# Kernel optimization log

Hardware: AMD Instinct MI355X
Metric: run time of the kernel (lower is better)

## Reference

```python
import jax, jax.numpy as jnp
import numpy as np

D = 1024
H = 16
DH = D // H
DFF = 4096
EPS = 1e-5


def new_gelu(u):
    # HF NewGELUActivation: 0.5*u*(1+tanh(sqrt(2/pi)*(u+0.044715*u^3)))
    c = np.sqrt(2.0 / np.pi).astype(np.float32)
    return 0.5 * u * (1.0 + jnp.tanh(c * (u + 0.044715 * u ** 3)))


def layer_norm(u, g, b):
    mu = jnp.mean(u, axis=-1, keepdims=True)
    var = jnp.mean((u - mu) ** 2, axis=-1, keepdims=True)
    return (u - mu) * jax.lax.rsqrt(var + EPS) * g + b


def setup_inputs() -> dict:
    key = jax.random.key(0)
    ks = jax.random.split(key, 12)
    s = 0.02
    inp = {
        "x": jax.random.normal(ks[0], (4, 1024, D), dtype=jnp.float32),
        "Wq": jax.random.normal(ks[1], (D, D), dtype=jnp.float32) * s,
        "bq": jnp.zeros((D,), jnp.float32),
        "Wk": jax.random.normal(ks[2], (D, D), dtype=jnp.float32) * s,
        "bk": jnp.zeros((D,), jnp.float32),
        "Wv": jax.random.normal(ks[3], (D, D), dtype=jnp.float32) * s,
        "bv": jnp.zeros((D,), jnp.float32),
        "Wo": jax.random.normal(ks[4], (D, D), dtype=jnp.float32) * s,
        "bo": jnp.zeros((D,), jnp.float32),
        "g1": jnp.ones((D,), jnp.float32),
        "b1": jnp.zeros((D,), jnp.float32),
        "W1": jax.random.normal(ks[5], (D, DFF), dtype=jnp.float32) * s,
        "bm1": jnp.zeros((DFF,), jnp.float32),
        "W2": jax.random.normal(ks[6], (DFF, D), dtype=jnp.float32) * s,
        "bm2": jnp.zeros((D,), jnp.float32),
        "g2": jnp.ones((D,), jnp.float32),
        "b2": jnp.zeros((D,), jnp.float32),
    }
    return inp


def reference(x, Wq, bq, Wk, bk, Wv, bv, Wo, bo, g1, b1, W1, bm1, W2, bm2, g2, b2):
    B, S, _ = x.shape
    q = (x @ Wq + bq).reshape(B, S, H, DH)
    k = (x @ Wk + bk).reshape(B, S, H, DH)
    v = (x @ Wv + bv).reshape(B, S, H, DH)
    scores = jnp.einsum("bshd,bthd->bhst", q, k) / np.sqrt(DH).astype(np.float32)
    probs = jax.nn.softmax(scores, axis=-1)
    attn = jnp.einsum("bhst,bthd->bshd", probs, v).reshape(B, S, D)
    attn = attn @ Wo + bo
    x1 = layer_norm(x + attn, g1, b1)
    mlp = new_gelu(x1 @ W1 + bm1) @ W2 + bm2
    out = layer_norm(x1 + mlp, g2, b2)
    return out
```

## Files before the change

### kernel.cpp

```cpp
#include <hip/hip_runtime.h>

#define D_    1024
#define HH    16
#define DHEAD 64
#define DFF_  4096
#define NTOK  4096
#define SQLEN 1024

typedef unsigned short ushort_t;
typedef __attribute__((ext_vector_type(8))) short short8;
typedef __attribute__((ext_vector_type(4))) float floatx4;

#define LOG2E 1.44269504f

__device__ __forceinline__ unsigned short f2bf(float f) {
  union { float f; unsigned u; } x; x.f = f;
  unsigned r = x.u + 0x7fffu + ((x.u >> 16) & 1u);
  return (unsigned short)(r >> 16);
}
__device__ __forceinline__ float bf2f(unsigned short u) {
  union { unsigned u; float f; } x; x.u = ((unsigned)u) << 16;
  return x.f;
}
__device__ __forceinline__ unsigned pack2bf_fast(float a, float b) {
  union { float f; unsigned u; } x, y; x.f = a; y.f = b;
  return __builtin_amdgcn_perm(y.u + 0x8000u, x.u + 0x8000u, 0x07060302u);
}
__device__ __forceinline__ float fast_exp2(float x) {
  return __builtin_amdgcn_exp2f(x);
}
__device__ __forceinline__ float fast_gelu(float u) {
  float u2 = u * u;
  float arg = u * (2.30220414f + 0.10294307f * u2);
  float e = __builtin_amdgcn_exp2f(arg);
  float r = __builtin_amdgcn_rcpf(e + 1.0f);
  return u - u * r;
}

__device__ __forceinline__ void async_ld16(const void* g, void* l) {
  __builtin_amdgcn_global_load_lds(
      (const __attribute__((address_space(1))) unsigned int*)g,
      (__attribute__((address_space(3))) unsigned int*)l, 16, 0, 0);
}

__device__ __forceinline__ unsigned lds_off(const void* p) {
  return (unsigned)(unsigned long long)
      (const __attribute__((address_space(3))) char*)p;
}

__global__ __launch_bounds__(256) void prep_kernel(
    const float* __restrict__ x, const float* __restrict__ Wq,
    const float* __restrict__ Wk, const float* __restrict__ Wv,
    const float* __restrict__ Wo, const float* __restrict__ W1,
    const float* __restrict__ W2,
    ushort_t* __restrict__ xb, ushort_t* __restrict__ wqkvt,
    ushort_t* __restrict__ wot, ushort_t* __restrict__ w1t,
    ushort_t* __restrict__ w2t) {
  int bid = blockIdx.x, tid = threadIdx.x;
  if (bid < 4096) {
    int i = bid * 256 + tid;
    float4 v = ((const float4*)x)[i];
    ushort4 o;
    o.x = f2bf(v.x); o.y = f2bf(v.y); o.z = f2bf(v.z); o.w = f2bf(v.w);
    ((ushort4*)xb)[i] = o;
    return;
  }
  __shared__ float tile[32][33];
  const float* W; ushort_t* T; int K, N, n0, k0;
  if (bid < 8192) {
    int id = bid - 4096, z = id >> 10, xy = id & 1023;
    W = (z == 0) ? Wq : (z == 1) ? Wk : (z == 2) ? Wv : Wo;
    T = (z < 3) ? wqkvt + (size_t)z * D_ * D_ : wot;
    K = D_; N = D_;
    n0 = (xy & 31) * 32; k0 = (xy >> 5) * 32;
  } else if (bid < 12288) {
    int id = bid - 8192;
    W = W1; T = w1t; K = D_; N = DFF_;
    n0 = (id & 127) * 32; k0 = (id >> 7) * 32;
  } else {
    int id = bid - 12288;
    W = W2; T = w2t; K = DFF_; N = D_;
    n0 = (id & 31) * 32; k0 = (id >> 5) * 32;
  }
  int tx = tid & 31, ty = tid >> 5;
#pragma unroll
  for (int i = 0; i < 4; i++)
    tile[ty + i * 8][tx] = W[(size_t)(k0 + ty + i * 8) * N + n0 + tx];
  __syncthreads();
#pragma unroll
  for (int i = 0; i < 4; i++)
    T[(size_t)(n0 + ty + i * 8) * K + k0 + tx] = f2bf(tile[tx][ty + i * 8]);
}

template <int MODE>
__global__ __launch_bounds__(512, 2) void gemm256(
    const ushort_t* __restrict__ A, const ushort_t* __restrict__ Bt,
    int M, int N, int K, int Ks, int nb,
    const float* __restrict__ bias0, const float* __restrict__ bias1,
    const float* __restrict__ bias2,
    ushort_t* __restrict__ o0, ushort_t* __restrict__ o1, ushort_t* __restrict__ o2) {
  __shared__ alignas(128) ushort_t sA[2][2][128 * 64];
  __shared__ alignas(128) ushort_t sB[2][2][128 * 64];
  int tid = threadIdx.x;
  int w = tid >> 6, lane = tid & 63, quad = lane >> 4, l16 = lane & 15;
  int wm = w >> 2, wn = w & 3;

  int sp = blockIdx.x / nb;
  int bid = blockIdx.x - sp * nb;
  int gridN = N >> 8;
  int Tn = nb >> 3;
  int lin = (bid & 7) * Tn + (bid >> 3);
  int ng = gridN << 3;
  int gidx = lin / ng;
  int rem = lin - gidx * ng;
  int m0 = ((gidx << 3) + (rem & 7)) << 8;
  int n0 = (rem >> 3) << 8;
  int kbeg = sp * Ks;
  int nkt = Ks >> 6;

  floatx4 acc[8][4];
#pragma unroll
  for (int i = 0; i < 8; i++)
#pragma unroll
    for (int j = 0; j < 4; j++) acc[i][j] = (floatx4){0.f, 0.f, 0.f, 0.f};

  int s8  = tid >> 3;
  int lcx = (tid & 7) ^ (s8 & 7);
  const ushort_t* gA = A + (size_t)(m0 + s8) * K + kbeg + lcx * 8;
  const ushort_t* gB = Bt + (size_t)(n0 + (s8 & 31) + (s8 >> 5) * 64) * K + kbeg + lcx * 8;
  char* sta = (char*)&sA[0][0][0] + w * 1024;
  char* stb = (char*)&sB[0][0][0] + w * 1024;

  unsigned kof0 = (unsigned)((quad ^ (l16 & 7)) << 4);
  unsigned vA  = lds_off(&sA[0][0][0]) + (unsigned)((wm * 64 + l16) * 128) + kof0;
  unsigned vAx = vA ^ 64u;
  unsigned vB  = lds_off(&sB[0][0][0]) + (unsigned)((wn * 32 + l16) * 128) + kof0;
  unsigned vBx = vB ^ 64u;

#define STG_A(db, h, ko) { const ushort_t* _g = gA + (size_t)(h) * 64 * K + (ko); \
    char* _l = sta + (db) * 32768 + (h) * 16384; \
    async_ld16(_g, _l); async_ld16(_g + (size_t)128 * K, _l + 8192); }
#define STG_B(db, h, ko) { const ushort_t* _g = gB + (size_t)(h) * 32 * K + (ko); \
    char* _l = stb + (db) * 32768 + (h) * 16384; \
    async_ld16(_g, _l); async_ld16(_g + (size_t)128 * K, _l + 8192); }
#define DSR(d, bs, lit) asm volatile("ds_read_b128 %0, %1 offset:" lit \
    : "=v"(d) : "v"(bs))
#define LDSA_G(L0, L1, L2, L3) { \
    DSR(a[0][0], vA, L0); DSR(a[0][1], vAx, L0); \
    DSR(a[1][0], vA, L1); DSR(a[1][1], vAx, L1); \
    DSR(a[2][0], vA, L2); DSR(a[2][1], vAx, L2); \
    DSR(a[3][0], vA, L3); DSR(a[3][1], vAx, L3); }
#define LDSB_G(DST, L0, L1) { \
    DSR(DST[0][0], vB, L0); DSR(DST[0][1], vBx, L0); \
    DSR(DST[1][0], vB, L1); DSR(DST[1][1], vBx, L1); }
#define MFMAQ(mq, nq, B_) { \
    _Pragma("unroll") for (int kc = 0; kc < 2; kc++) \
    _Pragma("unroll") for (int mt = 0; mt < 4; mt++) \
    _Pragma("unroll") for (int nt = 0; nt < 2; nt++) \
      acc[(mq) * 4 + mt][(nq) * 2 + nt] = __builtin_amdgcn_mfma_f32_16x16x32_bf16( \
          a[mt][kc], B_[nt][kc], acc[(mq) * 4 + mt][(nq) * 2 + nt], 0, 0, 0); }
#define BAR __builtin_amdgcn_s_barrier()
#define LGK0 { asm volatile("s_waitcnt lgkmcnt(0)" ::: "memory"); \
               __builtin_amdgcn_sched_barrier(0); }
#define VMW0 asm volatile("s_waitcnt vmcnt(0)" ::: "memory")
#define PRIO1 __builtin_amdgcn_s_setprio(1)
#define PRIO0 __builtin_amdgcn_s_setprio(0)
#define GTILE(A00, A01, A02, A03, A10, A11, A12, A13, B00, B01, B10, B11) { \
    LDSA_G(A00, A01, A02, A03); LDSB_G(b0, B00, B01); LDSB_G(b1, B10, B11); \
    LGK0; PRIO1; MFMAQ(0, 0, b0); MFMAQ(0, 1, b1); PRIO0; \
    LDSA_G(A10, A11, A12, A13); \
    LGK0; PRIO1; MFMAQ(1, 1, b1); MFMAQ(1, 0, b0); PRIO0; }
#define GTILE0 GTILE("0", "2048", "4096", "6144", \
                     "16384", "18432", "20480", "22528", \
                     "0", "2048", "16384", "18432")
#define GTILE1 GTILE("32768", "34816", "36864", "38912", \
                     "49152", "51200", "53248", "55296", \
                     "32768", "34816", "49152", "51200")

  short8 a[4][2], b0[2][2], b1[2][2];

  STG_A(0, 0, 0); STG_B(0, 0, 0); STG_B(0, 1, 0); STG_A(0, 1, 0);
  VMW0; BAR;

  for (int kt = 0; kt + 2 < nkt; kt += 2) {
    int ko1 = (kt + 1) << 6, ko2 = (kt + 2) << 6;
    STG_A(1, 0, ko1); STG_B(1, 0, ko1); STG_B(1, 1, ko1); STG_A(1, 1, ko1);
    GTILE0;
    VMW0; BAR;
    STG_A(0, 0, ko2); STG_B(0, 0, ko2); STG_B(0, 1, ko2); STG_A(0, 1, ko2);
    GTILE1;
    VMW0; BAR;
  }
  {
    int ko1 = (nkt - 1) << 6;
    STG_A(1, 0, ko1); STG_B(1, 0, ko1); STG_B(1, 1, ko1); STG_A(1, 1, ko1);
    GTILE0;
    VMW0; BAR;
    GTILE1;
  }

  if (MODE == 0) {
#pragma unroll
    for (int bj = 0; bj < 4; bj++) {
      int cg = n0 + wn * 64 + (bj >> 1) * 32 + (bj & 1) * 16 + l16;
      int sel = cg >> 10, nn = cg & 1023;
      const float* bpp = (sel == 0) ? bias0 : ((sel == 1) ? bias1 : bias2);
      float bb = bpp[nn];
      int hh = nn >> 6, dd = nn & 63;
#pragma unroll
      for (int ai = 0; ai < 8; ai++) {
        int rg0 = m0 + wm * 128 + (ai >> 2) * 64 + (ai & 3) * 16 + quad * 4;
        int b0_ = rg0 >> 10, s0 = rg0 & 1023;
        if (sel == 2) {
          ushort4 ov;
          ov.x = f2bf(acc[ai][bj][0] + bb);
          ov.y = f2bf(acc[ai][bj][1] + bb);
          ov.z = f2bf(acc[ai][bj][2] + bb);
          ov.w = f2bf(acc[ai][bj][3] + bb);
          *(ushort4*)(o2 + ((size_t)(b0_ * HH + hh) * DHEAD + dd) * SQLEN + s0) = ov;
        } else {
          ushort_t* dst = sel ? o1 : o0;
          float sc = (sel == 0) ? (0.125f * LOG2E) : 1.0f;
#pragma unroll
          for (int r = 0; r < 4; r++)
            dst[((size_t)(b0_ * HH + hh) * SQLEN + s0 + r) * DHEAD + dd] =
                f2bf((acc[ai][bj][r] + bb) * sc);
        }
      }
    }
  } else {
    size_t rowbase = (size_t)(m0 + wm * 128 + quad * 4) * N + (n0 + wn * 64 + l16);
    if (MODE == 3) rowbase += (size_t)sp * M * N;
    float bb[4];
    if (MODE == 2) {
#pragma unroll
      for (int c = 0; c < 4; c++)
        bb[c] = bias0[(n0 + wn * 64 + c * 16 + l16) & (N - 1)];
    }
#pragma unroll
    for (int ai = 0; ai < 8; ai++) {
#pragma unroll
      for (int r = 0; r < 4; r++) {
        ushort_t* pr = o0 + rowbase + (size_t)((ai >> 2) * 64 + (ai & 3) * 16 + r) * N;
        if (MODE == 2) {
          pr[0]  = f2bf(fast_gelu(acc[ai][0][r] + bb[0]));
          pr[16] = f2bf(fast_gelu(acc[ai][1][r] + bb[1]));
          pr[32] = f2bf(fast_gelu(acc[ai][2][r] + bb[2]));
          pr[48] = f2bf(fast_gelu(acc[ai][3][r] + bb[3]));
        } else {
          pr[0]  = f2bf(acc[ai][0][r]);
          pr[16] = f2bf(acc[ai][1][r]);
          pr[32] = f2bf(acc[ai][2][r]);
          pr[48] = f2bf(acc[ai][3][r]);
        }
      }
    }
  }
#undef STG_A
#undef STG_B
#undef DSR
#undef LDSA_G
#undef LDSB_G
#undef MFMAQ
#undef BAR
#undef LGK0
#undef VMW0
#undef PRIO1
#undef PRIO0
#undef GTILE
#undef GTILE0
#undef GTILE1
}

__global__ __launch_bounds__(256) void flash_attn_kernel(const ushort_t* __restrict__ q,
                                                         const ushort_t* __restrict__ k,
                                                         const ushort_t* __restrict__ vt,
                                                         ushort_t* __restrict__ ctx) {
  __shared__ alignas(16) ushort_t sQ[2][128 * 32];
  __shared__ alignas(16) ushort_t sK[2][64 * 32];
  __shared__ alignas(16) ushort_t sVt[2][64 * 32];
  __shared__ alignas(16) char sP[4][2][2][16 * 80];
  int tid = threadIdx.x;
  int w = tid >> 6, lane = tid & 63, quad = lane >> 4, l16 = lane & 15;
  int bh = blockIdx.x, qt = blockIdx.y;
  int b_ = bh >> 4, h_ = bh & 15;

  const ushort_t* Qp = q + ((size_t)bh * SQLEN + qt * 128) * DHEAD;
  const ushort_t* Kp = k + (size_t)bh * SQLEN * DHEAD;
  const ushort_t* Vtp = vt + (size_t)bh * DHEAD * SQLEN;

  int srow = lane >> 2, scol8 = (lane & 3) * 8;

#pragma unroll
  for (int h = 0; h < 2; h++)
#pragma unroll
    for (int p = 0; p < 2; p++)
      async_ld16(Qp + (h * 64 + w * 16 + srow) * 64 + p * 32 + scol8,
                 (char*)sQ + p * 8192 + (h * 64 + w * 16) * 64);

  float l_run[2] = {0.f, 0.f};
  floatx4 o_acc[2][4];
#pragma unroll
  for (int g = 0; g < 2; g++)
#pragma unroll
    for (int dt = 0; dt < 4; dt++) o_acc[g][dt] = (floatx4){0.f, 0.f, 0.f, 0.f};

  for (int kt = 0; kt < 16; kt++) {
    __syncthreads();
#pragma unroll
    for (int t = 0; t < 2; t++) {
      int id = w * 2 + t, panel = id & 1, rg = id >> 1;
      int row = rg * 16 + srow, col = panel * 32 + scol8;
      async_ld16(Kp + kt * 64 * 64 + row * 64 + col,
                 (char*)sK + panel * 4096 + rg * 1024);
      async_ld16(Vtp + (size_t)row * SQLEN + kt * 64 + col,
                 (char*)sVt + panel * 4096 + rg * 1024);
    }
    __syncthreads();

    floatx4 st[2][4];
#pragma unroll
    for (int g = 0; g < 2; g++)
#pragma unroll
      for (int nt = 0; nt < 4; nt++) st[g][nt] = (floatx4){0.f, 0.f, 0.f, 0.f};
#pragma unroll
    for (int kc = 0; kc < 2; kc++) {
      short8 aq0 = *(const short8*)(sQ[kc] + (w * 32 + l16) * 32 + quad * 8);
      short8 aq1 = *(const short8*)(sQ[kc] + (w * 32 + 16 + l16) * 32 + quad * 8);
#pragma unroll
      for (int nt = 0; nt < 4; nt++) {
        short8 kf = *(const short8*)(sK[kc] + (nt * 16 + l16) * 32 + quad * 8);
        st[0][nt] = __builtin_amdgcn_mfma_f32_16x16x32_bf16(kf, aq0, st[0][nt], 0, 0, 0);
        st[1][nt] = __builtin_amdgcn_mfma_f32_16x16x32_bf16(kf, aq1, st[1][nt], 0, 0, 0);
      }
    }

#pragma unroll
    for (int g = 0; g < 2; g++) {
#pragma unroll
      for (int nt = 0; nt < 4; nt++) {
        float p0 = fast_exp2(st[g][nt][0]);
        float p1 = fast_exp2(st[g][nt][1]);
        float p2 = fast_exp2(st[g][nt][2]);
        float p3 = fast_exp2(st[g][nt][3]);
        l_run[g] += (p0 + p1) + (p2 + p3);
        uint2 d2;
        d2.x = pack2bf_fast(p0, p1);
        d2.y = pack2bf_fast(p2, p3);
        *(uint2*)(&sP[w][g][nt >> 1][0] + l16 * 80 + (nt & 1) * 32 + quad * 8) = d2;
      }
    }

#pragma unroll
    for (int kc = 0; kc < 2; kc++) {
      short8 pf0 = *(const short8*)(&sP[w][0][kc][0] + l16 * 80 + quad * 16);
      short8 pf1 = *(const short8*)(&sP[w][1][kc][0] + l16 * 80 + quad * 16);
#pragma unroll
      for (int dt = 0; dt < 4; dt++) {
        short8 vf = *(const short8*)(sVt[kc] + (dt * 16 + l16) * 32 + quad * 8);
        o_acc[0][dt] = __builtin_amdgcn_mfma_f32_16x16x32_bf16(vf, pf0, o_acc[0][dt], 0, 0, 0);
        o_acc[1][dt] = __builtin_amdgcn_mfma_f32_16x16x32_bf16(vf, pf1, o_acc[1][dt], 0, 0, 0);
      }
    }
  }

#pragma unroll
  for (int g = 0; g < 2; g++) {
    float l = l_run[g];
    l += __shfl_xor(l, 16);
    l += __shfl_xor(l, 32);
    float inv = 1.f / fmaxf(l, 1e-30f);
    int s_ = qt * 128 + w * 32 + g * 16 + l16;
    ushort_t* cp = ctx + (size_t)(b_ * SQLEN + s_) * D_ + h_ * DHEAD + quad * 4;
#pragma unroll
    for (int dt = 0; dt < 4; dt++) {
      ushort4 ov;
      ov.x = f2bf(o_acc[g][dt][0] * inv);
      ov.y = f2bf(o_acc[g][dt][1] * inv);
      ov.z = f2bf(o_acc[g][dt][2] * inv);
      ov.w = f2bf(o_acc[g][dt][3] * inv);
      *(ushort4*)(cp + dt * 16) = ov;
    }
  }
}

template <int S, int WB>
__global__ __launch_bounds__(256) void ln_red_kernel(
    const ushort_t* __restrict__ parts, const float* __restrict__ bias,
    const float* __restrict__ res, const float* __restrict__ g,
    const float* __restrict__ b, float* __restrict__ outf,
    ushort_t* __restrict__ outb) {
  int row = blockIdx.x, tid = threadIdx.x;
  float4 v = ((const float4*)(res + (size_t)row * D_))[tid];
  float4 bb = ((const float4*)bias)[tid];
  v.x += bb.x; v.y += bb.y; v.z += bb.z; v.w += bb.w;
#pragma unroll
  for (int s = 0; s < S; s++) {
    ushort4 p = ((const ushort4*)(parts + (size_t)s * NTOK * D_ + (size_t)row * D_))[tid];
    v.x += bf2f(p.x); v.y += bf2f(p.y); v.z += bf2f(p.z); v.w += bf2f(p.w);
  }
  float s1 = v.x + v.y + v.z + v.w;
  float s2 = v.x * v.x + v.y * v.y + v.z * v.z + v.w * v.w;
#pragma unroll
  for (int off = 32; off > 0; off >>= 1) {
    s1 += __shfl_down(s1, off);
    s2 += __shfl_down(s2, off);
  }
  __shared__ float red[10];
  int wid = tid >> 6, lane = tid & 63;
  if (lane == 0) { red[wid] = s1; red[4 + wid] = s2; }
  __syncthreads();
  if (tid == 0) {
    float ts = red[0] + red[1] + red[2] + red[3];
    float ts2 = red[4] + red[5] + red[6] + red[7];
    float mu = ts * (1.f / 1024.f);
    float var = ts2 * (1.f / 1024.f) - mu * mu;
    red[8] = mu;
    red[9] = rsqrtf(var + 1e-5f);
  }
  __syncthreads();
  float mu = red[8], rsg = red[9];
  float4 gv = ((const float4*)g)[tid];
  float4 bv = ((const float4*)b)[tid];
  float4 o;
  o.x = (v.x - mu) * rsg * gv.x + bv.x;
  o.y = (v.y - mu) * rsg * gv.y + bv.y;
  o.z = (v.z - mu) * rsg * gv.z + bv.z;
  o.w = (v.w - mu) * rsg * gv.w + bv.w;
  if (outf) ((float4*)(outf + (size_t)row * D_))[tid] = o;
  if (WB) {
    ushort4 ob;
    ob.x = f2bf(o.x); ob.y = f2bf(o.y); ob.z = f2bf(o.z); ob.w = f2bf(o.w);
    ((ushort4*)(outb + (size_t)row * D_))[tid] = ob;
  }
}

extern "C" void kernel_launch(void* const* d_in, const int* in_sizes, int n_in,
                              void* d_out, int out_size, void* d_ws, size_t ws_size,
                              hipStream_t stream) {
  const float* x   = (const float*)d_in[0];
  const float* Wq  = (const float*)d_in[1];
  const float* bq  = (const float*)d_in[2];
  const float* Wk  = (const float*)d_in[3];
  const float* bk  = (const float*)d_in[4];
  const float* Wv  = (const float*)d_in[5];
  const float* bv  = (const float*)d_in[6];
  const float* Wo  = (const float*)d_in[7];
  const float* bo  = (const float*)d_in[8];
  const float* g1  = (const float*)d_in[9];
  const float* b1  = (const float*)d_in[10];
  const float* W1  = (const float*)d_in[11];
  const float* bm1 = (const float*)d_in[12];
  const float* W2  = (const float*)d_in[13];
  const float* bm2 = (const float*)d_in[14];
  const float* g2  = (const float*)d_in[15];
  const float* b2  = (const float*)d_in[16];
  float* out = (float*)d_out;

  char* ws = (char*)d_ws;
  const size_t MB = 1024 * 1024;
  ushort_t* xb    = (ushort_t*)(ws + 0);
  ushort_t* wqkvt = (ushort_t*)(ws + 8 * MB);
  ushort_t* wot   = (ushort_t*)(ws + 14 * MB);
  ushort_t* w1t   = (ushort_t*)(ws + 16 * MB);
  ushort_t* w2t   = (ushort_t*)(ws + 24 * MB);
  ushort_t* qb    = (ushort_t*)(ws + 32 * MB);
  ushort_t* kb    = (ushort_t*)(ws + 40 * MB);
  ushort_t* vtb   = (ushort_t*)(ws + 48 * MB);
  ushort_t* ctx   = (ushort_t*)(ws + 56 * MB);
  float*    x1    = (float*)   (ws + 64 * MB);
  ushort_t* x1b   = (ushort_t*)(ws + 80 * MB);
  ushort_t* hbuf  = (ushort_t*)(ws + 88 * MB);
  ushort_t* pWo   = (ushort_t*)(ws + 88 * MB);
  ushort_t* pMd   = (ushort_t*)(ws + 32 * MB);
  (void)ws_size; (void)in_sizes; (void)n_in; (void)out_size;

  hipLaunchKernelGGL(prep_kernel, dim3(16384), dim3(256), 0, stream,
                     x, Wq, Wk, Wv, Wo, W1, W2, xb, wqkvt, wot, w1t, w2t);

  hipLaunchKernelGGL((gemm256<0>), dim3(192), dim3(512), 0, stream,
                     xb, wqkvt, NTOK, 3072, D_, 1024, 192, bq, bk, bv, qb, kb, vtb);

  hipLaunchKernelGGL(flash_attn_kernel, dim3(4 * HH, SQLEN / 128), dim3(256), 0, stream,
                     qb, kb, vtb, ctx);

  hipLaunchKernelGGL((gemm256<3>), dim3(256), dim3(512), 0, stream,
                     ctx, wot, NTOK, D_, D_, 256, 64,
                     (const float*)nullptr, (const float*)nullptr,
                     (const float*)nullptr, pWo, (ushort_t*)nullptr, (ushort_t*)nullptr);

  hipLaunchKernelGGL((ln_red_kernel<4, 1>), dim3(NTOK), dim3(256), 0, stream,
                     pWo, bo, x, g1, b1, x1, x1b);

  hipLaunchKernelGGL((gemm256<2>), dim3(256), dim3(512), 0, stream,
                     x1b, w1t, NTOK, DFF_, D_, 1024, 256, bm1, (const float*)nullptr,
                     (const float*)nullptr, hbuf, (ushort_t*)nullptr, (ushort_t*)nullptr);

  hipLaunchKernelGGL((gemm256<3>), dim3(256), dim3(512), 0, stream,
                     hbuf, w2t, NTOK, D_, DFF_, 1024, 64,
                     (const float*)nullptr, (const float*)nullptr,
                     (const float*)nullptr, pMd, (ushort_t*)nullptr, (ushort_t*)nullptr);

  hipLaunchKernelGGL((ln_red_kernel<4, 0>), dim3(NTOK), dim3(256), 0, stream,
                     pMd, bm2, x1, g2, b2, out, (ushort_t*)nullptr);
}
```

Before: 319.6 us.

## Rework 256x256 GEMM to 4 waves with 128x128 warp tiles

The GEMM block goes from 8 waves (each a 128x64 sub-tile) to 4 waves, each computing a 128x128 sub-tile, so every wave holds 8x8 accumulator fragments. LDS staging becomes contiguous 256-row tiles with a single-stage loop that flips double buffers, and partial lgkmcnt waits let MFMAs start before all LDS reads finish. The aim is more operand reuse per LDS read and less per-wave overhead. The cost is much higher register pressure (256 accumulator VGPRs plus operands), fewer waves available to hide latency, and possible spills.

```diff
diff --git a/kernel.cpp b/kernel.cpp
--- a/kernel.cpp
+++ b/kernel.cpp
@@ -93,17 +93,17 @@
 }
 
 template <int MODE>
-__global__ __launch_bounds__(512, 2) void gemm256(
+__global__ __launch_bounds__(256, 1) void gemm256(
     const ushort_t* __restrict__ A, const ushort_t* __restrict__ Bt,
     int M, int N, int K, int Ks, int nb,
     const float* __restrict__ bias0, const float* __restrict__ bias1,
     const float* __restrict__ bias2,
     ushort_t* __restrict__ o0, ushort_t* __restrict__ o1, ushort_t* __restrict__ o2) {
-  __shared__ alignas(128) ushort_t sA[2][2][128 * 64];
-  __shared__ alignas(128) ushort_t sB[2][2][128 * 64];
+  __shared__ alignas(128) ushort_t sA[2][256 * 64];
+  __shared__ alignas(128) ushort_t sB[2][256 * 64];
   int tid = threadIdx.x;
   int w = tid >> 6, lane = tid & 63, quad = lane >> 4, l16 = lane & 15;
-  int wm = w >> 2, wn = w & 3;
+  int wm = w >> 1, wn = w & 1;
 
   int sp = blockIdx.x / nb;
   int bid = blockIdx.x - sp * nb;
@@ -118,98 +118,94 @@
   int kbeg = sp * Ks;
   int nkt = Ks >> 6;
 
-  floatx4 acc[8][4];
+  floatx4 acc[8][8];
 #pragma unroll
   for (int i = 0; i < 8; i++)
 #pragma unroll
-    for (int j = 0; j < 4; j++) acc[i][j] = (floatx4){0.f, 0.f, 0.f, 0.f};
+    for (int j = 0; j < 8; j++) acc[i][j] = (floatx4){0.f, 0.f, 0.f, 0.f};
 
   int s8  = tid >> 3;
   int lcx = (tid & 7) ^ (s8 & 7);
   const ushort_t* gA = A + (size_t)(m0 + s8) * K + kbeg + lcx * 8;
-  const ushort_t* gB = Bt + (size_t)(n0 + (s8 & 31) + (s8 >> 5) * 64) * K + kbeg + lcx * 8;
-  char* sta = (char*)&sA[0][0][0] + w * 1024;
-  char* stb = (char*)&sB[0][0][0] + w * 1024;
+  const ushort_t* gB = Bt + (size_t)(n0 + s8) * K + kbeg + lcx * 8;
+  char* sta = (char*)&sA[0][0] + w * 1024;
+  char* stb = (char*)&sB[0][0] + w * 1024;
 
   unsigned kof0 = (unsigned)((quad ^ (l16 & 7)) << 4);
-  unsigned vA  = lds_off(&sA[0][0][0]) + (unsigned)((wm * 64 + l16) * 128) + kof0;
+  unsigned vA  = lds_off(&sA[0][0]) + (unsigned)((wm * 128 + l16) * 128) + kof0;
   unsigned vAx = vA ^ 64u;
-  unsigned vB  = lds_off(&sB[0][0][0]) + (unsigned)((wn * 32 + l16) * 128) + kof0;
+  unsigned vB  = lds_off(&sB[0][0]) + (unsigned)((wn * 128 + l16) * 128) + kof0;
   unsigned vBx = vB ^ 64u;
 
-#define STG_A(db, h, ko) { const ushort_t* _g = gA + (size_t)(h) * 64 * K + (ko); \
-    char* _l = sta + (db) * 32768 + (h) * 16384; \
-    async_ld16(_g, _l); async_ld16(_g + (size_t)128 * K, _l + 8192); }
-#define STG_B(db, h, ko) { const ushort_t* _g = gB + (size_t)(h) * 32 * K + (ko); \
-    char* _l = stb + (db) * 32768 + (h) * 16384; \
-    async_ld16(_g, _l); async_ld16(_g + (size_t)128 * K, _l + 8192); }
+#define STG_TILE(db, ko) { \
+    _Pragma("unroll") for (int j = 0; j < 8; j++) \
+      async_ld16(gA + (size_t)j * 32 * K + (ko), sta + (db) * 32768 + j * 4096); \
+    _Pragma("unroll") for (int j = 0; j < 8; j++) \
+      async_ld16(gB + (size_t)j * 32 * K + (ko), stb + (db) * 32768 + j * 4096); }
 #define DSR(d, bs, lit) asm volatile("ds_read_b128 %0, %1 offset:" lit \
     : "=v"(d) : "v"(bs))
-#define LDSA_G(L0, L1, L2, L3) { \
-    DSR(a[0][0], vA, L0); DSR(a[0][1], vAx, L0); \
-    DSR(a[1][0], vA, L1); DSR(a[1][1], vAx, L1); \
-    DSR(a[2][0], vA, L2); DSR(a[2][1], vAx, L2); \
-    DSR(a[3][0], vA, L3); DSR(a[3][1], vAx, L3); }
-#define LDSB_G(DST, L0, L1) { \
-    DSR(DST[0][0], vB, L0); DSR(DST[0][1], vBx, L0); \
-    DSR(DST[1][0], vB, L1); DSR(DST[1][1], vBx, L1); }
-#define MFMAQ(mq, nq, B_) { \
+#define LDA_H0 { DSR(aP[0][0], vA, "0");     DSR(aP[0][1], vAx, "0"); \
+                 DSR(aP[1][0], vA, "2048");  DSR(aP[1][1], vAx, "2048"); \
+                 DSR(aP[2][0], vA, "4096");  DSR(aP[2][1], vAx, "4096"); \
+                 DSR(aP[3][0], vA, "6144");  DSR(aP[3][1], vAx, "6144"); }
+#define LDA_H1 { DSR(aQ[0][0], vA, "8192");  DSR(aQ[0][1], vAx, "8192"); \
+                 DSR(aQ[1][0], vA, "10240"); DSR(aQ[1][1], vAx, "10240"); \
+                 DSR(aQ[2][0], vA, "12288"); DSR(aQ[2][1], vAx, "12288"); \
+                 DSR(aQ[3][0], vA, "14336"); DSR(aQ[3][1], vAx, "14336"); }
+#define LDB_ALL { DSR(b[0][0], vB, "0");     DSR(b[0][1], vBx, "0"); \
+                  DSR(b[1][0], vB, "2048");  DSR(b[1][1], vBx, "2048"); \
+                  DSR(b[2][0], vB, "4096");  DSR(b[2][1], vBx, "4096"); \
+                  DSR(b[3][0], vB, "6144");  DSR(b[3][1], vBx, "6144"); \
+                  DSR(b[4][0], vB, "8192");  DSR(b[4][1], vBx, "8192"); \
+                  DSR(b[5][0], vB, "10240"); DSR(b[5][1], vBx, "10240"); \
+                  DSR(b[6][0], vB, "12288"); DSR(b[6][1], vBx, "12288"); \
+                  DSR(b[7][0], vB, "14336"); DSR(b[7][1], vBx, "14336"); }
+#define MFMAC(AS, mh, NL, NH) { \
     _Pragma("unroll") for (int kc = 0; kc < 2; kc++) \
     _Pragma("unroll") for (int mt = 0; mt < 4; mt++) \
-    _Pragma("unroll") for (int nt = 0; nt < 2; nt++) \
-      acc[(mq) * 4 + mt][(nq) * 2 + nt] = __builtin_amdgcn_mfma_f32_16x16x32_bf16( \
-          a[mt][kc], B_[nt][kc], acc[(mq) * 4 + mt][(nq) * 2 + nt], 0, 0, 0); }
+    _Pragma("unroll") for (int nt = (NL); nt < (NH); nt++) \
+      acc[(mh) * 4 + mt][nt] = __builtin_amdgcn_mfma_f32_16x16x32_bf16( \
+          AS[mt][kc], b[nt][kc], acc[(mh) * 4 + mt][nt], 0, 0, 0); }
 #define BAR __builtin_amdgcn_s_barrier()
-#define LGK0 { asm volatile("s_waitcnt lgkmcnt(0)" ::: "memory"); \
-               __builtin_amdgcn_sched_barrier(0); }
+#define LGKC(n) { asm volatile("s_waitcnt lgkmcnt(" #n ")" ::: "memory"); \
+                  __builtin_amdgcn_sched_barrier(0); }
 #define VMW0 asm volatile("s_waitcnt vmcnt(0)" ::: "memory")
 #define PRIO1 __builtin_amdgcn_s_setprio(1)
 #define PRIO0 __builtin_amdgcn_s_setprio(0)
-#define GTILE(A00, A01, A02, A03, A10, A11, A12, A13, B00, B01, B10, B11) { \
-    LDSA_G(A00, A01, A02, A03); LDSB_G(b0, B00, B01); LDSB_G(b1, B10, B11); \
-    LGK0; PRIO1; MFMAQ(0, 0, b0); MFMAQ(0, 1, b1); PRIO0; \
-    LDSA_G(A10, A11, A12, A13); \
-    LGK0; PRIO1; MFMAQ(1, 1, b1); MFMAQ(1, 0, b0); PRIO0; }
-#define GTILE0 GTILE("0", "2048", "4096", "6144", \
-                     "16384", "18432", "20480", "22528", \
-                     "0", "2048", "16384", "18432")
-#define GTILE1 GTILE("32768", "34816", "36864", "38912", \
-                     "49152", "51200", "53248", "55296", \
-                     "32768", "34816", "49152", "51200")
-
-  short8 a[4][2], b0[2][2], b1[2][2];
-
-  STG_A(0, 0, 0); STG_B(0, 0, 0); STG_B(0, 1, 0); STG_A(0, 1, 0);
+#define FLIPBUF { vA ^= 32768u; vAx ^= 32768u; vB ^= 32768u; vBx ^= 32768u; }
+#define GTILE { \
+    LDA_H0; LDB_ALL; \
+    LGKC(8);  PRIO1; MFMAC(aP, 0, 0, 4); PRIO0; \
+    LDA_H1; \
+    LGKC(8);  PRIO1; MFMAC(aP, 0, 4, 8); PRIO0; \
+    LGKC(0);  PRIO1; MFMAC(aQ, 1, 0, 4); MFMAC(aQ, 1, 4, 8); PRIO0; }
+
+  short8 aP[4][2], aQ[4][2], b[8][2];
+
+  STG_TILE(0, 0);
   VMW0; BAR;
 
-  for (int kt = 0; kt + 2 < nkt; kt += 2) {
-    int ko1 = (kt + 1) << 6, ko2 = (kt + 2) << 6;
-    STG_A(1, 0, ko1); STG_B(1, 0, ko1); STG_B(1, 1, ko1); STG_A(1, 1, ko1);
-    GTILE0;
+  for (int kt = 0; kt < nkt - 1; kt++) {
+    int dn = (kt + 1) & 1;
+    int ko = (kt + 1) << 6;
+    STG_TILE(dn, ko);
+    GTILE;
     VMW0; BAR;
-    STG_A(0, 0, ko2); STG_B(0, 0, ko2); STG_B(0, 1, ko2); STG_A(0, 1, ko2);
-    GTILE1;
-    VMW0; BAR;
-  }
-  {
-    int ko1 = (nkt - 1) << 6;
-    STG_A(1, 0, ko1); STG_B(1, 0, ko1); STG_B(1, 1, ko1); STG_A(1, 1, ko1);
-    GTILE0;
-    VMW0; BAR;
-    GTILE1;
-  }
+    FLIPBUF;
+  }
+  GTILE;
 
   if (MODE == 0) {
 #pragma unroll
-    for (int bj = 0; bj < 4; bj++) {
-      int cg = n0 + wn * 64 + (bj >> 1) * 32 + (bj & 1) * 16 + l16;
+    for (int bj = 0; bj < 8; bj++) {
+      int cg = n0 + wn * 128 + bj * 16 + l16;
       int sel = cg >> 10, nn = cg & 1023;
       const float* bpp = (sel == 0) ? bias0 : ((sel == 1) ? bias1 : bias2);
       float bb = bpp[nn];
       int hh = nn >> 6, dd = nn & 63;
 #pragma unroll
       for (int ai = 0; ai < 8; ai++) {
-        int rg0 = m0 + wm * 128 + (ai >> 2) * 64 + (ai & 3) * 16 + quad * 4;
+        int rg0 = m0 + wm * 128 + ai * 16 + quad * 4;
         int b0_ = rg0 >> 10, s0 = rg0 & 1023;
         if (sel == 2) {
           ushort4 ov;
@@ -229,47 +225,44 @@
       }
     }
   } else {
-    size_t rowbase = (size_t)(m0 + wm * 128 + quad * 4) * N + (n0 + wn * 64 + l16);
+    size_t rowbase = (size_t)(m0 + wm * 128 + quad * 4) * N + (n0 + wn * 128 + l16);
     if (MODE == 3) rowbase += (size_t)sp * M * N;
-    float bb[4];
+    float bb[8];
     if (MODE == 2) {
 #pragma unroll
-      for (int c = 0; c < 4; c++)
-        bb[c] = bias0[(n0 + wn * 64 + c * 16 + l16) & (N - 1)];
+      for (int c = 0; c < 8; c++)
+        bb[c] = bias0[(n0 + wn * 128 + c * 16 + l16) & (N - 1)];
     }
 #pragma unroll
     for (int ai = 0; ai < 8; ai++) {
 #pragma unroll
       for (int r = 0; r < 4; r++) {
-        ushort_t* pr = o0 + rowbase + (size_t)((ai >> 2) * 64 + (ai & 3) * 16 + r) * N;
+        ushort_t* pr = o0 + rowbase + (size_t)(ai * 16 + r) * N;
         if (MODE == 2) {
-          pr[0]  = f2bf(fast_gelu(acc[ai][0][r] + bb[0]));
-          pr[16] = f2bf(fast_gelu(acc[ai][1][r] + bb[1]));
-          pr[32] = f2bf(fast_gelu(acc[ai][2][r] + bb[2]));
-          pr[48] = f2bf(fast_gelu(acc[ai][3][r] + bb[3]));
+#pragma unroll
+          for (int bj = 0; bj < 8; bj++)
+            pr[bj * 16] = f2bf(fast_gelu(acc[ai][bj][r] + bb[bj]));
         } else {
-          pr[0]  = f2bf(acc[ai][0][r]);
-          pr[16] = f2bf(acc[ai][1][r]);
-          pr[32] = f2bf(acc[ai][2][r]);
-          pr[48] = f2bf(acc[ai][3][r]);
+#pragma unroll
+          for (int bj = 0; bj < 8; bj++)
+            pr[bj * 16] = f2bf(acc[ai][bj][r]);
         }
       }
     }
   }
-#undef STG_A
-#undef STG_B
+#undef STG_TILE
 #undef DSR
-#undef LDSA_G
-#undef LDSB_G
-#undef MFMAQ
+#undef LDA_H0
+#undef LDA_H1
+#undef LDB_ALL
+#undef MFMAC
 #undef BAR
-#undef LGK0
+#undef LGKC
 #undef VMW0
 #undef PRIO1
 #undef PRIO0
+#undef FLIPBUF
 #undef GTILE
-#undef GTILE0
-#undef GTILE1
 }
 
 __global__ __launch_bounds__(256) void flash_attn_kernel(const ushort_t* __restrict__ q,
@@ -478,13 +471,13 @@
   hipLaunchKernelGGL(prep_kernel, dim3(16384), dim3(256), 0, stream,
                      x, Wq, Wk, Wv, Wo, W1, W2, xb, wqkvt, wot, w1t, w2t);
 
-  hipLaunchKernelGGL((gemm256<0>), dim3(192), dim3(512), 0, stream,
+  hipLaunchKernelGGL((gemm256<0>), dim3(192), dim3(256), 0, stream,
                      xb, wqkvt, NTOK, 3072, D_, 1024, 192, bq, bk, bv, qb, kb, vtb);
 
   hipLaunchKernelGGL(flash_attn_kernel, dim3(4 * HH, SQLEN / 128), dim3(256), 0, stream,
                      qb, kb, vtb, ctx);
 
-  hipLaunchKernelGGL((gemm256<3>), dim3(256), dim3(512), 0, stream,
+  hipLaunchKernelGGL((gemm256<3>), dim3(256), dim3(256), 0, stream,
                      ctx, wot, NTOK, D_, D_, 256, 64,
                      (const float*)nullptr, (const float*)nullptr,
                      (const float*)nullptr, pWo, (ushort_t*)nullptr, (ushort_t*)nullptr);
@@ -492,11 +485,11 @@
   hipLaunchKernelGGL((ln_red_kernel<4, 1>), dim3(NTOK), dim3(256), 0, stream,
                      pWo, bo, x, g1, b1, x1, x1b);
 
-  hipLaunchKernelGGL((gemm256<2>), dim3(256), dim3(512), 0, stream,
+  hipLaunchKernelGGL((gemm256<2>), dim3(256), dim3(256), 0, stream,
                      x1b, w1t, NTOK, DFF_, D_, 1024, 256, bm1, (const float*)nullptr,
                      (const float*)nullptr, hbuf, (ushort_t*)nullptr, (ushort_t*)nullptr);
 
-  hipLaunchKernelGGL((gemm256<3>), dim3(256), dim3(512), 0, stream,
+  hipLaunchKernelGGL((gemm256<3>), dim3(256), dim3(256), 0, stream,
                      hbuf, w2t, NTOK, D_, DFF_, 1024, 64,
                      (const float*)nullptr, (const float*)nullptr,
                      (const float*)nullptr, pMd, (ushort_t*)nullptr, (ushort_t*)nullptr);
```

Measured after the change: 345.5 us. 8.1% more time.
